# Optimization experiments

Hardware: AMD Instinct MI355X
Metric: run time of the kernel (lower is better)

The kernel has to match this reference:

```python
import jax, jax.numpy as jnp
import numpy as np


def setup_inputs() -> dict:
    key = jax.random.key(0)
    k1, k2 = jax.random.split(key)
    B, S, H, D = 4, 2048, 12, 64
    v = jax.random.normal(k1, (B, S, H, D), dtype=jnp.float32)
    # learned per-head positional weights, sorted ascending along last dim
    # (mirrors torch.sort(torch.randn(H, S), dim=-1)[0])
    w = jnp.sort(jax.random.normal(k2, (H, S), dtype=jnp.float32), axis=-1)
    return {"v": v, "w": w}


def reference(v, w):
    # PositionalBias._naive
    # v: [B, S, H, D]; w: [H, S_max]
    B, S, H, D = v.shape
    seq_len = S - 2  # v[:, 1:-1] is the non-special-token span
    w_ = w[:, :seq_len]  # [H, seq_len]
    # _construct_bias builds bias[h, l, j] = w[h, |l - j|] (symmetric Toeplitz)
    pos = jnp.arange(seq_len)
    idx = jnp.abs(pos[:, None] - pos[None, :])  # [seq_len, seq_len]
    bias = w_[:, idx]  # [H, seq_len, seq_len]
    # zero-pad one row/col on each side -> [H, S, S]
    bias = jnp.pad(bias, ((0, 0), (1, 1), (1, 1)))
    # z_pb: [1, S, H]
    z_pb = jnp.sum(bias, axis=-1).T[None, :, :]
    # pbv: [B, S, H, D]
    pbv = jnp.einsum('nlhd,hlj->njhd', v, bias)
    return (pbv, z_pb)
```

## Files before the change

kernel.cpp:

```cpp
#include <hip/hip_runtime.h>
#include <hip/hip_bf16.h>


typedef short short8 __attribute__((ext_vector_type(8)));
typedef float floatx4 __attribute__((ext_vector_type(4)));

#define QN 4352

__device__ __attribute__((aligned(16))) short g_vt[4 * 12 * 64 * 2048];
__device__ __attribute__((aligned(16))) short g_wt[12 * QN * 8];

__device__ __forceinline__ unsigned short f2bf(float f) {
  union { __hip_bfloat16 b; unsigned short u; } cv;
  cv.b = __float2bfloat16(f);
  return cv.u;
}

__global__ __launch_bounds__(256) void prep_kernel(const float* __restrict__ v,
                                                   const float* __restrict__ w,
                                                   float* __restrict__ out) {
  __shared__ float zls[4096];
  __shared__ float wsum[4];

  const int bx  = blockIdx.x;
  const int tid = threadIdx.x;

  if (bx >= 1548) {
    const int h = bx - 1548;
    const float* wh = w + (size_t)h * 2048;
    short* F = g_wt + (size_t)h * QN * 8;
    for (int q = tid; q < QN; q += 256) {
      unsigned short buf[8] __attribute__((aligned(16)));
      #pragma unroll
      for (int i = 0; i < 8; ++i) {
        int t = 2174 - q - i;
        int a = t < 0 ? -t : t;
        buf[i] = (a <= 2045) ? f2bf(wh[a]) : (unsigned short)0;
      }
      *(short8*)&F[(size_t)q * 8] = *(const short8*)buf;
    }
    return;
  }

  if (bx >= 1536) {
    const int h = bx - 1536;
    float* wvv = zls;
    float* pfx = zls + 2048;
    const float* wh = w + (size_t)h * 2048;
    float* zout = out + 6291456;
    for (int i = tid; i < 2048; i += 256) wvv[i] = (i < 2046) ? wh[i] : 0.f;
    __syncthreads();
    const int base = tid * 8;
    float run0 = 0.f;
    #pragma unroll
    for (int k = 0; k < 8; ++k) run0 += wvv[base + k];
    float x = run0;
    #pragma unroll
    for (int dd = 1; dd < 64; dd <<= 1) {
      float y = __shfl_up(x, dd);
      if ((tid & 63) >= dd) x += y;
    }
    if ((tid & 63) == 63) wsum[tid >> 6] = x;
    __syncthreads();
    const int wid4 = tid >> 6;
    float woff = 0.f;
    #pragma unroll
    for (int u = 0; u < 3; ++u) { float t = wsum[u]; if (u < wid4) woff += t; }
    float pr = x + woff - run0;
    #pragma unroll
    for (int k = 0; k < 8; ++k) { pr += wvv[base + k]; pfx[base + k] = pr; }
    __syncthreads();
    for (int i = tid; i < 2046; i += 256) {
      float z = pfx[i] + pfx[2045 - i] - wvv[0];
      zout[(size_t)(i + 1) * 12 + h] = z;
    }
    if (tid == 0) { zout[h] = 0.f; zout[(size_t)2047 * 12 + h] = 0.f; }
    return;
  }

  const int chunk = bx & 31;
  const int slice = bx >> 5;
  const int n = slice / 12, h = slice - n * 12;
  const int lane = tid & 63;
  const int wv   = tid >> 6;
  const int l0 = chunk * 64 + wv * 16;

  const float* src = v + (((size_t)n * 2048 + l0) * 12 + h) * 64 + lane;
  short* dst = g_vt + (((size_t)n * 12 + h) * 64 + lane) * 2048 + l0;

  float f[16];
  #pragma unroll
  for (int k = 0; k < 16; ++k) f[k] = src[(size_t)k * 768];
  #pragma unroll
  for (int g = 0; g < 2; ++g) {
    short8 b;
    #pragma unroll
    for (int i = 0; i < 8; ++i) {
      int l = l0 + g * 8 + i;
      b[i] = (l == 0 || l == 2047) ? (short)0 : (short)f2bf(f[g * 8 + i]);
    }
    *(short8*)&dst[g * 8] = b;
  }
}

__global__ __launch_bounds__(256, 3) void gemm_kernel(float* __restrict__ out) {
  __shared__ __attribute__((aligned(16))) short Als[2304 * 8];

  const int bx  = blockIdx.x;
  const int tid = threadIdx.x;

  const int slice = bx % 48;
  const int jt    = bx / 48;
  const int ndt = slice & 3;
  const int h   = slice >> 2;
  const int lane = tid & 63;
  const int wid  = tid >> 6;
  const int lm = lane & 15, quad = lane >> 4;
  const int jb = jt * 128;
  const int d  = wid * 16 + lm;

  const short* vtb = g_vt + (((size_t)ndt * 12 + h) * 64 + d) * 2048;
  auto load_bf = [&](int lb) -> short8 {
    return *(const short8*)&vtb[lb];
  };

  short8 bc0 = load_bf(quad * 8);
  short8 bc1 = load_bf(32 + quad * 8);
  short8 bn0 = load_bf(64 + quad * 8);
  short8 bn1 = load_bf(96 + quad * 8);

  const short* wsrc = g_wt + (size_t)h * QN * 8 + (size_t)(2047 - jb) * 8;
  #pragma unroll
  for (int k = 0; k < 9; ++k) {
    *(short8*)&Als[(size_t)(k * 256 + tid) * 8] =
        *(const short8*)&wsrc[(size_t)(k * 256 + tid) * 8];
  }
  __syncthreads();

  const int abase = 127 + quad * 8 - lm;
  auto load_af = [&](int p) -> short8 {
    return *(const short8*)&Als[(size_t)(p + abase) * 8];
  };

  short8 afr[10];
  #pragma unroll
  for (int i = 0; i < 10; ++i) afr[i] = load_af((i - 7) * 16);

  floatx4 acc[8];
  #pragma unroll
  for (int ma = 0; ma < 8; ++ma) acc[ma] = (floatx4){0.f, 0.f, 0.f, 0.f};

  #pragma unroll 4
  for (int t = 0; t < 32; ++t) {
    const int l0 = t * 64;
    int t2 = t + 2; if (t2 > 31) t2 = 31;
    const int lb = t2 * 64 + quad * 8;
    short8 bm0 = load_bf(lb);
    short8 bm1 = load_bf(lb + 32);
    const int l0n = (t < 31) ? l0 + 64 : l0;
    short8 na0 = load_af(l0n - 16);
    short8 na1 = load_af(l0n);
    short8 na2 = load_af(l0n + 16);
    short8 na3 = load_af(l0n + 32);

    __builtin_amdgcn_s_setprio(1);
    #pragma unroll
    for (int ma = 0; ma < 8; ++ma)
      acc[ma] = __builtin_amdgcn_mfma_f32_16x16x32_bf16(afr[7 - ma], bc0, acc[ma], 0, 0, 0);
    #pragma unroll
    for (int ma = 0; ma < 8; ++ma)
      acc[ma] = __builtin_amdgcn_mfma_f32_16x16x32_bf16(afr[9 - ma], bc1, acc[ma], 0, 0, 0);
    __builtin_amdgcn_s_setprio(0);

    #pragma unroll
    for (int i = 0; i < 6; ++i) afr[i] = afr[i + 4];
    afr[6] = na0; afr[7] = na1; afr[8] = na2; afr[9] = na3;
    bc0 = bn0; bc1 = bn1;
    bn0 = bm0; bn1 = bm1;
  }

  float* obase = out + (size_t)ndt * 1572864 + (size_t)h * 64 + d;
  #pragma unroll
  for (int ma = 0; ma < 8; ++ma) {
    floatx4 cc = acc[ma];
    #pragma unroll
    for (int r = 0; r < 4; ++r) {
      int j = jb + ma * 16 + quad * 4 + r;
      float val = (j == 0 || j == 2047) ? 0.f : cc[r];
      obase[(size_t)j * 768] = val;
    }
  }
}

extern "C" void kernel_launch(void* const* d_in, const int* in_sizes, int n_in,
                              void* d_out, int out_size, void* d_ws, size_t ws_size,
                              hipStream_t stream) {
  const float* v = (const float*)d_in[0];
  const float* w = (const float*)d_in[1];
  float* out = (float*)d_out;
  prep_kernel<<<dim3(1560), 256, 0, stream>>>(v, w, out);
  gemm_kernel<<<dim3(768), 256, 0, stream>>>(out);
}
```

Before: 122.1 us.

## Transpose v through LDS in prep kernel and raise gemm occupancy bound

The v-to-bf16 transpose now stages packed bf16 pairs in a padded shared-memory tile, so each thread writes contiguous 64-byte runs of the transposed buffer instead of scattered 16-byte stores per lane. Each block covers 128 positions instead of 64, which halves the prep grid. Separately, the gemm kernel's launch bounds move from 3 to 4 waves per SIMD, which may push the compiler to limit registers and risk spills.

```diff
diff --git a/kernel.cpp b/kernel.cpp
--- a/kernel.cpp
+++ b/kernel.cpp
@@ -4,6 +4,7 @@
 
 typedef short short8 __attribute__((ext_vector_type(8)));
 typedef float floatx4 __attribute__((ext_vector_type(4)));
+typedef unsigned uint4_ __attribute__((ext_vector_type(4)));
 
 #define QN 4352
 
@@ -19,14 +20,15 @@
 __global__ __launch_bounds__(256) void prep_kernel(const float* __restrict__ v,
                                                    const float* __restrict__ w,
                                                    float* __restrict__ out) {
+  __shared__ unsigned tls[64 * 65];
   __shared__ float zls[4096];
   __shared__ float wsum[4];
 
   const int bx  = blockIdx.x;
   const int tid = threadIdx.x;
 
-  if (bx >= 1548) {
-    const int h = bx - 1548;
+  if (bx >= 780) {
+    const int h = bx - 780;
     const float* wh = w + (size_t)h * 2048;
     short* F = g_wt + (size_t)h * QN * 8;
     for (int q = tid; q < QN; q += 256) {
@@ -42,8 +44,8 @@
     return;
   }
 
-  if (bx >= 1536) {
-    const int h = bx - 1536;
+  if (bx >= 768) {
+    const int h = bx - 768;
     float* wvv = zls;
     float* pfx = zls + 2048;
     const float* wh = w + (size_t)h * 2048;
@@ -78,32 +80,40 @@
     return;
   }
 
-  const int chunk = bx & 31;
-  const int slice = bx >> 5;
+  const int chunk = bx & 15;
+  const int slice = bx >> 4;
   const int n = slice / 12, h = slice - n * 12;
   const int lane = tid & 63;
   const int wv   = tid >> 6;
-  const int l0 = chunk * 64 + wv * 16;
-
-  const float* src = v + (((size_t)n * 2048 + l0) * 12 + h) * 64 + lane;
-  short* dst = g_vt + (((size_t)n * 12 + h) * 64 + lane) * 2048 + l0;
-
-  float f[16];
-  #pragma unroll
-  for (int k = 0; k < 16; ++k) f[k] = src[(size_t)k * 768];
-  #pragma unroll
-  for (int g = 0; g < 2; ++g) {
-    short8 b;
-    #pragma unroll
-    for (int i = 0; i < 8; ++i) {
-      int l = l0 + g * 8 + i;
-      b[i] = (l == 0 || l == 2047) ? (short)0 : (short)f2bf(f[g * 8 + i]);
-    }
-    *(short8*)&dst[g * 8] = b;
-  }
-}
-
-__global__ __launch_bounds__(256, 3) void gemm_kernel(float* __restrict__ out) {
+  const int lbase = chunk * 128 + wv * 32;
+
+  const float* src = v + (((size_t)n * 2048 + lbase) * 12 + h) * 64 + lane;
+  #pragma unroll
+  for (int kk = 0; kk < 16; ++kk) {
+    float f0 = src[(size_t)(2 * kk)     * 768];
+    float f1 = src[(size_t)(2 * kk + 1) * 768];
+    int l = lbase + 2 * kk;
+    unsigned lo = (l == 0)        ? 0u : (unsigned)f2bf(f0);
+    unsigned hi = (l + 1 == 2047) ? 0u : (unsigned)f2bf(f1);
+    tls[lane * 65 + wv * 16 + kk] = lo | (hi << 16);
+  }
+  __syncthreads();
+
+  const int r = tid >> 2;
+  const int m = tid & 3;
+  unsigned xbuf[16];
+  #pragma unroll
+  for (int k = 0; k < 16; ++k) xbuf[k] = tls[r * 65 + m * 16 + k];
+  unsigned* dstu = (unsigned*)(g_vt + (((size_t)n * 12 + h) * 64 + r) * 2048 +
+                               (size_t)chunk * 128) + m * 16;
+  #pragma unroll
+  for (int k4 = 0; k4 < 4; ++k4) {
+    uint4_ val = {xbuf[k4 * 4], xbuf[k4 * 4 + 1], xbuf[k4 * 4 + 2], xbuf[k4 * 4 + 3]};
+    *(uint4_*)&dstu[k4 * 4] = val;
+  }
+}
+
+__global__ __launch_bounds__(256, 4) void gemm_kernel(float* __restrict__ out) {
   __shared__ __attribute__((aligned(16))) short Als[2304 * 8];
 
   const int bx  = blockIdx.x;
@@ -198,6 +208,6 @@
   const float* v = (const float*)d_in[0];
   const float* w = (const float*)d_in[1];
   float* out = (float*)d_out;
-  prep_kernel<<<dim3(1560), 256, 0, stream>>>(v, w, out);
+  prep_kernel<<<dim3(792), 256, 0, stream>>>(v, w, out);
   gemm_kernel<<<dim3(768), 256, 0, stream>>>(out);
 }
```

Result: no change. 122.4 us (+0.3%).
